# Performance work log

Hardware: AMD Instinct MI355X
Metric: run time of the kernel (lower is better)

Reference implementation:

```python
import jax, jax.numpy as jnp
import numpy as np

EMBED_DIM = 512
N_HEAD = 8
HEAD_DIM = EMBED_DIM // N_HEAD  # 64
B, S = 2, 4096
NEG_FILL = -1e20


def setup_inputs() -> dict:
    key = jax.random.key(0)
    ks = jax.random.split(key, 9)
    inp = {
        "key": jax.random.normal(ks[0], (B, S, EMBED_DIM), jnp.float32),
        "query": jax.random.normal(ks[1], (B, S, EMBED_DIM), jnp.float32),
        "value": jax.random.normal(ks[2], (B, S, EMBED_DIM), jnp.float32),
        "mask": jax.random.randint(ks[3], (1, 1, S, S), 0, 2, jnp.int32),
        # per-head projections (shared across heads, as in the source: a single
        # d x d nn.Linear applied to the last dim of [B,S,H,d])
        "Wq": jax.random.normal(ks[4], (HEAD_DIM, HEAD_DIM), jnp.float32) / np.sqrt(HEAD_DIM),
        "Wk": jax.random.normal(ks[5], (HEAD_DIM, HEAD_DIM), jnp.float32) / np.sqrt(HEAD_DIM),
        "Wv": jax.random.normal(ks[6], (HEAD_DIM, HEAD_DIM), jnp.float32) / np.sqrt(HEAD_DIM),
        "Wo": jax.random.normal(ks[7], (EMBED_DIM, EMBED_DIM), jnp.float32) / np.sqrt(EMBED_DIM),
        "bo": jax.random.normal(ks[8], (EMBED_DIM,), jnp.float32) * 0.01,
    }
    return inp


def reference(key, query, value, mask, Wq, Wk, Wv, Wo, bo):
    b, sq, e = query.shape
    skv = key.shape[1]
    h, d = N_HEAD, HEAD_DIM
    # split heads: [B, S, H, d]
    q = query.reshape(b, sq, h, d) @ Wq.T
    k = key.reshape(b, skv, h, d) @ Wk.T
    v = value.reshape(b, skv, h, d) @ Wv.T
    # scores: [B, H, Sq, Skv]
    scores = jnp.einsum("bqhd,bkhd->bhqk", q, k)
    # source masks BEFORE scaling: fill -1e20 then divide by sqrt(d)
    scores = jnp.where(mask == 0, NEG_FILL, scores)
    scores = scores / np.sqrt(d).astype(np.float32)
    attn = jax.nn.softmax(scores, axis=-1)
    ctx = jnp.einsum("bhqk,bkhd->bqhd", attn, v)  # [B, Sq, H, d]
    concat = ctx.reshape(b, sq, h * d)
    return concat @ Wo.T + bo
```

## Files before the change

### kernel.cpp

```cpp
#include <hip/hip_runtime.h>

typedef __bf16 bf16;
typedef __attribute__((ext_vector_type(8)))  bf16     bf16x8;
typedef __attribute__((ext_vector_type(4)))  bf16     bf16x4;
typedef __attribute__((ext_vector_type(16))) float    f32x16;
typedef __attribute__((ext_vector_type(4)))  float    f32x4;
typedef __attribute__((ext_vector_type(4)))  unsigned uint4v;
typedef __attribute__((ext_vector_type(2)))  unsigned uint2v;

#define SLEN 4096
#define NHEAD 8
#define HDIM 64
#define EMB 512
#define NTILES 64
#define SCALE_LOG2E 0.1803336100254854f

__device__ __forceinline__ f32x16 mfma32(bf16x8 a, bf16x8 b, f32x16 c) {
  return __builtin_amdgcn_mfma_f32_32x32x16_bf16(a, b, c, 0, 0, 0);
}

__device__ __forceinline__ void cp16(const void* g, const void* l) {
  __builtin_amdgcn_global_load_lds(
      (__attribute__((address_space(1))) unsigned int*)(unsigned long long)g,
      (__attribute__((address_space(3))) unsigned int*)(unsigned int)(unsigned long long)l,
      16, 0, 0);
}

__device__ __forceinline__ unsigned pk2(float a, float b) {
  unsigned short ua = __builtin_bit_cast(unsigned short, (bf16)a);
  unsigned short ub = __builtin_bit_cast(unsigned short, (bf16)b);
  return (unsigned)ua | ((unsigned)ub << 16);
}

__global__ __launch_bounds__(256, 2) void proj_qkv(
    const float* __restrict__ key, const float* __restrict__ query, const float* __restrict__ value,
    const float* __restrict__ Wq, const float* __restrict__ Wk, const float* __restrict__ Wv,
    bf16* __restrict__ Qb, bf16* __restrict__ Kb, bf16* __restrict__ VT)
{
  __shared__ __align__(16) bf16 tile[128][64];
  const int tid = threadIdx.x, w = tid >> 6, lane = tid & 63, l31 = lane & 31, lh = lane >> 5;
  const int r0 = blockIdx.x * 128;
  const int m0 = r0 + w * 32;

  #pragma unroll
  for (int p = 0; p < 3; ++p) {
    const float* X = (p == 0) ? query : (p == 1) ? key : value;
    const float* W = (p == 0) ? Wq    : (p == 1) ? Wk  : Wv;

    bf16x8 af[4];
    {
      const float* xr = X + (size_t)(m0 + l31) * 64 + 8 * lh;
      #pragma unroll
      for (int c = 0; c < 4; ++c) {
        f32x4 lo = *(const f32x4*)(xr + c * 16);
        f32x4 hi = *(const f32x4*)(xr + c * 16 + 4);
        bf16x8 v;
        #pragma unroll
        for (int j = 0; j < 4; ++j) { v[j] = (bf16)lo[j]; v[4 + j] = (bf16)hi[j]; }
        af[c] = v;
      }
    }
    bf16x8 bfr[2][4];
    #pragma unroll
    for (int nb = 0; nb < 2; ++nb) {
      const float* wr = W + (size_t)(l31 + 32 * nb) * 64 + 8 * lh;
      #pragma unroll
      for (int c = 0; c < 4; ++c) {
        f32x4 lo = *(const f32x4*)(wr + c * 16);
        f32x4 hi = *(const f32x4*)(wr + c * 16 + 4);
        bf16x8 v;
        #pragma unroll
        for (int j = 0; j < 4; ++j) { v[j] = (bf16)lo[j]; v[4 + j] = (bf16)hi[j]; }
        bfr[nb][c] = v;
      }
    }
    f32x16 a0, a1;
    #pragma unroll
    for (int r = 0; r < 16; ++r) { a0[r] = 0.f; a1[r] = 0.f; }
    #pragma unroll
    for (int c = 0; c < 4; ++c) {
      a0 = mfma32(af[c], bfr[0][c], a0);
      a1 = mfma32(af[c], bfr[1][c], a1);
    }

    __syncthreads();
    #pragma unroll
    for (int r = 0; r < 16; ++r) {
      const int row = w * 32 + (r & 3) + 8 * (r >> 2) + 4 * lh;
      tile[row][l31]      = (bf16)a0[r];
      tile[row][l31 + 32] = (bf16)a1[r];
    }
    __syncthreads();

    if (p < 2) {
      bf16* OUT = p ? Kb : Qb;
      const int rloc = tid >> 1, half = tid & 1;
      const int rg = r0 + rloc, bs = rg >> 3, h = rg & 7, b = bs >> 12, sidx = bs & 4095;
      bf16* dst = OUT + (((size_t)(b * 8 + h) * SLEN + sidx) * 64 + half * 32);
      const bf16* srcp = &tile[rloc][half * 32];
      #pragma unroll
      for (int u = 0; u < 4; ++u) *(uint4v*)(dst + u * 8) = *(const uint4v*)(srcp + u * 8);
    } else {
      const int h = tid >> 5, d0 = tid & 31;
      const int b = blockIdx.x >> 8, s0 = (blockIdx.x * 16) & 4095;
      #pragma unroll
      for (int dh = 0; dh < 2; ++dh) {
        const int dd = d0 + 32 * dh;
        unsigned pk4[8];
        #pragma unroll
        for (int t2 = 0; t2 < 8; ++t2) {
          unsigned short ua = __builtin_bit_cast(unsigned short, tile[(2 * t2) * 8 + h][dd]);
          unsigned short ub = __builtin_bit_cast(unsigned short, tile[(2 * t2 + 1) * 8 + h][dd]);
          pk4[t2] = (unsigned)ua | ((unsigned)ub << 16);
        }
        bf16* dst = VT + ((size_t)(b * 8 + h) * 64 + dd) * SLEN + s0;
        uint4v A; A[0] = pk4[0]; A[1] = pk4[1]; A[2] = pk4[2]; A[3] = pk4[3];
        uint4v Bv; Bv[0] = pk4[4]; Bv[1] = pk4[5]; Bv[2] = pk4[6]; Bv[3] = pk4[7];
        *(uint4v*)(dst) = A;
        *(uint4v*)(dst + 8) = Bv;
      }
    }
  }
}

__device__ __forceinline__ unsigned nib_compress(unsigned x) {
  x = (x | (x >> 4)) & 0x00FF00FFu;
  x = (x | (x >> 8)) & 0x0000FFFFu;
  return x;
}
__global__ void pack_mask(const int* __restrict__ mask, unsigned* __restrict__ MW)
{
  const int w = threadIdx.x >> 6, lane = threadIdx.x & 63;
  const int q = blockIdx.x * 4 + w;
  const int* row = mask + (size_t)q * SLEN;
  unsigned long long mine = 0ull;
  #pragma unroll 4
  for (int i = 0; i < 64; ++i) {
    unsigned long long b = __ballot(row[i * 64 + lane] != 0);
    if (i == lane) mine = b;
  }
  const unsigned lo = (unsigned)mine, hi = (unsigned)(mine >> 32);
  const unsigned w0 = nib_compress(lo & 0x0F0F0F0Fu)        | (nib_compress(hi & 0x0F0F0F0Fu) << 16);
  const unsigned w1 = nib_compress((lo >> 4) & 0x0F0F0F0Fu) | (nib_compress((hi >> 4) & 0x0F0F0F0Fu) << 16);
  MW[(size_t)lane * SLEN + q] = w0;
  MW[(size_t)NTILES * SLEN + (size_t)lane * SLEN + q] = w1;
}

__global__ void wo_split(const float* __restrict__ Wo, bf16* __restrict__ WH, bf16* __restrict__ WL)
{
  const int i = (blockIdx.x * 256 + threadIdx.x) * 4;
  f32x4 v = *(const f32x4*)(Wo + i);
  bf16x4 h, l;
  #pragma unroll
  for (int j = 0; j < 4; ++j) { h[j] = (bf16)v[j]; l[j] = (bf16)(v[j] - (float)h[j]); }
  *(bf16x4*)(WH + i) = h;
  *(bf16x4*)(WL + i) = l;
}

__device__ __forceinline__ void stage_kv4(const bf16* Kb, const bf16* VT, bf16* Kf, bf16* Vf,
                                          int bh, int kv0, int buf, int w, int l31, int lh)
{
  #pragma unroll
  for (int qq = 0; qq < 2; ++qq) {
    const int fid = w * 2 + qq, mb = fid >> 2, c = fid & 3;
    const bf16* ks = Kb + ((size_t)bh * SLEN + kv0 + 32 * mb + l31) * HDIM + c * 16 + 8 * lh;
    cp16(ks, Kf + buf * 4096 + fid * 512);
    const bf16* vs = VT + ((size_t)bh * HDIM + 32 * mb + l31) * SLEN + kv0 + c * 16 + 8 * lh;
    cp16(vs, Vf + buf * 4096 + fid * 512);
  }
}

__global__ __launch_bounds__(256, 4) void attn_kernel(
    const bf16* __restrict__ Qb, const bf16* __restrict__ Kb, const bf16* __restrict__ VT,
    const unsigned* __restrict__ MW,
    bf16* __restrict__ ctxh, bf16* __restrict__ ctxl)
{
  __shared__ __align__(16) unsigned char smem[32768];
  bf16* Kf = (bf16*)smem;
  bf16* Vf = (bf16*)(smem + 16384);

  const int tid = threadIdx.x, w = tid >> 6, lane = tid & 63, l31 = lane & 31, lh = lane >> 5;
  const int qg = w & 1, kc = w >> 1;
  const int bh = blockIdx.x >> 6, qt = blockIdx.x & 63;
  const int q0 = qt * 64;
  const int qrow = q0 + qg * 32 + l31;
  const int lh4 = 4 * lh;

  bf16x8 qf[4];
  {
    const bf16* qp = Qb + ((size_t)bh * SLEN + qrow) * HDIM + 8 * lh;
    #pragma unroll
    for (int c = 0; c < 4; ++c) qf[c] = *(const bf16x8*)(qp + c * 16);
  }

  f32x16 o0, o1;
  #pragma unroll
  for (int r = 0; r < 16; ++r) { o0[r] = 0.f; o1[r] = 0.f; }
  float ls0 = 0.f, ls1 = 0.f, ls2 = 0.f, ls3 = 0.f;

  stage_kv4(Kb, VT, Kf, Vf, bh, 0, 0, w, l31, lh);
  __syncthreads();

  const unsigned* MWl = MW + (size_t)lh * NTILES * SLEN;
  unsigned mw = MWl[qrow];
  for (int t = 0; t < NTILES; ++t) {
    const int cur = t & 1;
    if (t + 1 < NTILES) stage_kv4(Kb, VT, Kf, Vf, bh, (t + 1) * 64, cur ^ 1, w, l31, lh);
    unsigned mwn = 0u;
    if (t + 1 < NTILES) mwn = MWl[(size_t)(t + 1) * SLEN + qrow];

    f32x16 s;
    #pragma unroll
    for (int r = 0; r < 16; ++r) s[r] = 0.f;
    #pragma unroll
    for (int c = 0; c < 4; ++c) {
      bf16x8 a = *(const bf16x8*)(Kf + cur * 4096 + (kc * 4 + c) * 512 + lane * 8);
      s = mfma32(a, qf[c], s);
    }

    const unsigned mwk = mw >> (kc * 16);
    float p[16];
    #pragma unroll
    for (int r = 0; r < 16; ++r) {
      float e = __builtin_amdgcn_exp2f(s[r] * SCALE_LOG2E);
      e *= (float)((mwk >> r) & 1u);
      p[r] = e;
      if      ((r & 3) == 0) ls0 += e;
      else if ((r & 3) == 1) ls1 += e;
      else if ((r & 3) == 2) ls2 += e;
      else                   ls3 += e;
    }

    bf16x8 bp[2];
    #pragma unroll
    for (int cc = 0; cc < 2; ++cc) {
      const int rb = cc * 8;
      unsigned wA0 = pk2(p[rb + 0], p[rb + 1]);
      unsigned wA1 = pk2(p[rb + 2], p[rb + 3]);
      unsigned wB0 = pk2(p[rb + 4], p[rb + 5]);
      unsigned wB1 = pk2(p[rb + 6], p[rb + 7]);
      uint2v r0 = __builtin_amdgcn_permlane32_swap(wA0, wB0, false, false);
      uint2v r1 = __builtin_amdgcn_permlane32_swap(wA1, wB1, false, false);
      uint4v fw; fw[0] = r0[0]; fw[1] = r1[0]; fw[2] = r0[1]; fw[3] = r1[1];
      bp[cc] = __builtin_bit_cast(bf16x8, fw);
    }

    #pragma unroll
    for (int cc = 0; cc < 2; ++cc) {
      bf16x8 v0 = *(const bf16x8*)(Vf + cur * 4096 + (0 * 4 + kc * 2 + cc) * 512 + lane * 8);
      bf16x8 v1 = *(const bf16x8*)(Vf + cur * 4096 + (1 * 4 + kc * 2 + cc) * 512 + lane * 8);
      o0 = mfma32(v0, bp[cc], o0);
      o1 = mfma32(v1, bp[cc], o1);
    }

    __syncthreads();
    mw = mwn;
  }

  float plsum = (ls0 + ls1) + (ls2 + ls3);
  plsum += __shfl_xor(plsum, 32);

  float* PO = (float*)smem;
  float* PL = (float*)(smem + 16384);
  bf16*  Tr = (bf16*)(smem + 17408);

  if (w >= 2) {
    const int pw = w - 2;
    #pragma unroll
    for (int r = 0; r < 16; ++r) {
      PO[(pw * 32 + r) * 64 + lane]      = o0[r];
      PO[(pw * 32 + 16 + r) * 64 + lane] = o1[r];
    }
    PL[pw * 64 + lane] = plsum;
  }
  __syncthreads();

  if (w < 2) {
    #pragma unroll
    for (int r = 0; r < 16; ++r) {
      o0[r] += PO[(w * 32 + r) * 64 + lane];
      o1[r] += PO[(w * 32 + 16 + r) * 64 + lane];
    }
    plsum += PL[w * 64 + lane];
    const float inv = 1.f / plsum;
    #pragma unroll
    for (int r = 0; r < 16; ++r) { o0[r] *= inv; o1[r] *= inv; }
  }
  __syncthreads();

  if (w < 2) {
    #pragma unroll
    for (int r = 0; r < 16; ++r) {
      const int dr = (r & 3) + 8 * (r >> 2) + lh4;
      Tr[(w * 32 + l31) * 72 + dr]      = (bf16)o0[r];
      Tr[(w * 32 + l31) * 72 + 32 + dr] = (bf16)o1[r];
    }
  }
  __syncthreads();
  if (tid < 128) {
    const int rloc = tid >> 1, half = tid & 1;
    bf16* dst = ctxh + ((size_t)bh * SLEN + q0 + rloc) * 64 + half * 32;
    const bf16* srcp = Tr + rloc * 72 + half * 32;
    #pragma unroll
    for (int u = 0; u < 4; ++u) *(uint4v*)(dst + u * 8) = *(const uint4v*)(srcp + u * 8);
  }
  __syncthreads();
  if (w < 2) {
    #pragma unroll
    for (int r = 0; r < 16; ++r) {
      const int dr = (r & 3) + 8 * (r >> 2) + lh4;
      const float h0 = (float)(bf16)o0[r];
      const float h1 = (float)(bf16)o1[r];
      Tr[(w * 32 + l31) * 72 + dr]      = (bf16)(o0[r] - h0);
      Tr[(w * 32 + l31) * 72 + 32 + dr] = (bf16)(o1[r] - h1);
    }
  }
  __syncthreads();
  if (tid < 128) {
    const int rloc = tid >> 1, half = tid & 1;
    bf16* dst = ctxl + ((size_t)bh * SLEN + q0 + rloc) * 64 + half * 32;
    const bf16* srcp = Tr + rloc * 72 + half * 32;
    #pragma unroll
    for (int u = 0; u < 4; ++u) *(uint4v*)(dst + u * 8) = *(const uint4v*)(srcp + u * 8);
  }
}

__global__ __launch_bounds__(256, 2) void out_proj(
    const bf16* __restrict__ CH, const bf16* __restrict__ CL,
    const bf16* __restrict__ WH, const bf16* __restrict__ WL,
    const float* __restrict__ bo, float* __restrict__ out)
{
  __shared__ __align__(16) bf16 Af[2][4][4][64][8];
  const int tid = threadIdx.x, w = tid >> 6, lane = tid & 63, l31 = lane & 31, lh = lane >> 5;
  const int mt = blockIdx.x >> 3, nt = blockIdx.x & 7;
  const int bs0 = mt * 128, n0 = nt * 64;
  const int b = bs0 >> 12, sbase = bs0 & 4095;

  f32x16 a0, a1;
  #pragma unroll
  for (int r = 0; r < 16; ++r) { a0[r] = 0.f; a1[r] = 0.f; }

  for (int kk = 0; kk < 8; ++kk) {
    __syncthreads();
    #pragma unroll
    for (int qq = 0; qq < 8; ++qq) {
      const int fid = w * 8 + qq, pl = fid >> 4, mb = (fid >> 2) & 3, c = fid & 3;
      const bf16* src = (pl ? CL : CH) +
          ((size_t)(b * 8 + kk) * SLEN + sbase + 32 * mb + l31) * 64 + 16 * c + 8 * lh;
      cp16(src, &Af[pl][mb][c][0][0]);
    }
    __syncthreads();

    bf16x8 bh0[4], bl0[4], bh1[4], bl1[4], ah[4], al[4];
    #pragma unroll
    for (int c = 0; c < 4; ++c) {
      const size_t o0off = (size_t)(n0 + l31) * EMB + kk * 64 + 16 * c + 8 * lh;
      const size_t o1off = (size_t)(n0 + l31 + 32) * EMB + kk * 64 + 16 * c + 8 * lh;
      bh0[c] = *(const bf16x8*)(WH + o0off);
      bl0[c] = *(const bf16x8*)(WL + o0off);
      bh1[c] = *(const bf16x8*)(WH + o1off);
      bl1[c] = *(const bf16x8*)(WL + o1off);
      ah[c] = *(const bf16x8*)(&Af[0][w][c][lane][0]);
      al[c] = *(const bf16x8*)(&Af[1][w][c][lane][0]);
    }
    #pragma unroll
    for (int c = 0; c < 4; ++c) {
      a0 = mfma32(ah[c], bh0[c], a0);
      a0 = mfma32(ah[c], bl0[c], a0);
      a0 = mfma32(al[c], bh0[c], a0);
      a1 = mfma32(ah[c], bh1[c], a1);
      a1 = mfma32(ah[c], bl1[c], a1);
      a1 = mfma32(al[c], bh1[c], a1);
    }
  }

  const float bv0 = bo[n0 + l31], bv1 = bo[n0 + l31 + 32];
  #pragma unroll
  for (int r = 0; r < 16; ++r) {
    const int row = bs0 + w * 32 + (r & 3) + 8 * (r >> 2) + 4 * lh;
    out[(size_t)row * EMB + n0 + l31]      = a0[r] + bv0;
    out[(size_t)row * EMB + n0 + l31 + 32] = a1[r] + bv1;
  }
}

extern "C" void kernel_launch(void* const* d_in, const int* in_sizes, int n_in,
                              void* d_out, int out_size, void* d_ws, size_t ws_size,
                              hipStream_t stream)
{
  (void)in_sizes; (void)n_in; (void)out_size; (void)ws_size;
  const float* key   = (const float*)d_in[0];
  const float* query = (const float*)d_in[1];
  const float* value = (const float*)d_in[2];
  const int*   mask  = (const int*)d_in[3];
  const float* Wq    = (const float*)d_in[4];
  const float* Wk    = (const float*)d_in[5];
  const float* Wv    = (const float*)d_in[6];
  const float* Wo    = (const float*)d_in[7];
  const float* bo    = (const float*)d_in[8];
  float* out = (float*)d_out;

  char* ws = (char*)d_ws;
  bf16* Qb = (bf16*)(ws);
  bf16* Kb = (bf16*)(ws + (8ull  << 20));
  bf16* VT = (bf16*)(ws + (16ull << 20));
  unsigned* MW = (unsigned*)(ws + (24ull << 20));
  bf16* CH = (bf16*)(ws + (26ull << 20));
  bf16* CL = (bf16*)(ws + (34ull << 20));
  bf16* WH = (bf16*)(ws + (42ull << 20));
  bf16* WL = (bf16*)(ws + (42ull << 20) + (512ull << 10));

  proj_qkv<<<512, 256, 0, stream>>>(key, query, value, Wq, Wk, Wv, Qb, Kb, VT);
  pack_mask<<<1024, 256, 0, stream>>>(mask, MW);
  wo_split<<<256, 256, 0, stream>>>(Wo, WH, WL);
  attn_kernel<<<1024, 256, 0, stream>>>(Qb, Kb, VT, MW, CH, CL);
  out_proj<<<512, 256, 0, stream>>>(CH, CL, WH, WL, bo, out);
}
```

Measured before the change: 233.8 us.

## Split attention KV range across two blocks and combine partial results

The attention kernel can now split the key/value sequence into two halves processed by separate blocks. Each block writes unnormalised fp32 partial outputs and row sums to workspace, and a new combine kernel merges them into the hi/lo bf16 context. The softmax scale is folded into Q during projection, the mask multiply becomes a bitwise AND, and the tile loop is manually unrolled with pointer increments. The split mode turns on only when the workspace is large enough, and it adds extra global traffic and one more kernel launch.

```diff
diff --git a/kernel.cpp b/kernel.cpp
--- a/kernel.cpp
+++ b/kernel.cpp
@@ -9,7 +9,6 @@
 typedef __attribute__((ext_vector_type(2)))  unsigned uint2v;
 
 #define SLEN 4096
-#define NHEAD 8
 #define HDIM 64
 #define EMB 512
 #define NTILES 64
@@ -83,21 +82,22 @@
       a1 = mfma32(af[c], bfr[1][c], a1);
     }
 
+    const float qs = (p == 0) ? SCALE_LOG2E : 1.0f;
     __syncthreads();
     #pragma unroll
     for (int r = 0; r < 16; ++r) {
       const int row = w * 32 + (r & 3) + 8 * (r >> 2) + 4 * lh;
-      tile[row][l31]      = (bf16)a0[r];
-      tile[row][l31 + 32] = (bf16)a1[r];
+      tile[row][l31]      = (bf16)(a0[r] * qs);
+      tile[row][l31 + 32] = (bf16)(a1[r] * qs);
     }
     __syncthreads();
 
     if (p < 2) {
       bf16* OUT = p ? Kb : Qb;
-      const int rloc = tid >> 1, half = tid & 1;
+      const int rloc = tid >> 1, hf = tid & 1;
       const int rg = r0 + rloc, bs = rg >> 3, h = rg & 7, b = bs >> 12, sidx = bs & 4095;
-      bf16* dst = OUT + (((size_t)(b * 8 + h) * SLEN + sidx) * 64 + half * 32);
-      const bf16* srcp = &tile[rloc][half * 32];
+      bf16* dst = OUT + (((size_t)(b * 8 + h) * SLEN + sidx) * 64 + hf * 32);
+      const bf16* srcp = &tile[rloc][hf * 32];
       #pragma unroll
       for (int u = 0; u < 4; ++u) *(uint4v*)(dst + u * 8) = *(const uint4v*)(srcp + u * 8);
     } else {
@@ -157,171 +157,233 @@
   *(bf16x4*)(WL + i) = l;
 }
 
-__device__ __forceinline__ void stage_kv4(const bf16* Kb, const bf16* VT, bf16* Kf, bf16* Vf,
-                                          int bh, int kv0, int buf, int w, int l31, int lh)
-{
-  #pragma unroll
-  for (int qq = 0; qq < 2; ++qq) {
-    const int fid = w * 2 + qq, mb = fid >> 2, c = fid & 3;
-    const bf16* ks = Kb + ((size_t)bh * SLEN + kv0 + 32 * mb + l31) * HDIM + c * 16 + 8 * lh;
-    cp16(ks, Kf + buf * 4096 + fid * 512);
-    const bf16* vs = VT + ((size_t)bh * HDIM + 32 * mb + l31) * SLEN + kv0 + c * 16 + 8 * lh;
-    cp16(vs, Vf + buf * 4096 + fid * 512);
-  }
-}
-
 __global__ __launch_bounds__(256, 4) void attn_kernel(
     const bf16* __restrict__ Qb, const bf16* __restrict__ Kb, const bf16* __restrict__ VT,
     const unsigned* __restrict__ MW,
-    bf16* __restrict__ ctxh, bf16* __restrict__ ctxl)
+    bf16* __restrict__ ctxh, bf16* __restrict__ ctxl,
+    float* __restrict__ PO, float* __restrict__ PLg, int split)
 {
   __shared__ __align__(16) unsigned char smem[32768];
-  bf16* Kf = (bf16*)smem;
-  bf16* Vf = (bf16*)(smem + 16384);
+  unsigned char* const Ksm = smem;
+  unsigned char* const Vsm = smem + 16384;
 
   const int tid = threadIdx.x, w = tid >> 6, lane = tid & 63, l31 = lane & 31, lh = lane >> 5;
   const int qg = w & 1, kc = w >> 1;
-  const int bh = blockIdx.x >> 6, qt = blockIdx.x & 63;
+  const int half = blockIdx.x >> 10;
+  const int rem = blockIdx.x & 1023;
+  const int bh = rem >> 6, qt = rem & 63;
   const int q0 = qt * 64;
   const int qrow = q0 + qg * 32 + l31;
   const int lh4 = 4 * lh;
-
-  bf16x8 qf[4];
-  {
-    const bf16* qp = Qb + ((size_t)bh * SLEN + qrow) * HDIM + 8 * lh;
-    #pragma unroll
-    for (int c = 0; c < 4; ++c) qf[c] = *(const bf16x8*)(qp + c * 16);
-  }
-
-  f32x16 o0, o1;
-  #pragma unroll
-  for (int r = 0; r < 16; ++r) { o0[r] = 0.f; o1[r] = 0.f; }
-  float ls0 = 0.f, ls1 = 0.f, ls2 = 0.f, ls3 = 0.f;
-
-  stage_kv4(Kb, VT, Kf, Vf, bh, 0, 0, w, l31, lh);
+  const int kcs = kc << 4;
+  const int ntiles = (split == 2) ? 32 : 64;
+  const int kt0 = half * 32;
+
+  const bf16* qp = Qb + ((size_t)bh * SLEN + qrow) * HDIM + 8 * lh;
+  const bf16x8 qf0 = *(const bf16x8*)(qp);
+  const bf16x8 qf1 = *(const bf16x8*)(qp + 16);
+  const bf16x8 qf2 = *(const bf16x8*)(qp + 32);
+  const bf16x8 qf3 = *(const bf16x8*)(qp + 48);
+
+  const int f0 = 2 * w, f1 = 2 * w + 1;
+  const bf16* kp0 = Kb + ((size_t)bh * SLEN + kt0 * 64 + (f0 >> 2) * 32 + l31) * HDIM + (f0 & 3) * 16 + 8 * lh;
+  const bf16* kp1 = Kb + ((size_t)bh * SLEN + kt0 * 64 + (f1 >> 2) * 32 + l31) * HDIM + (f1 & 3) * 16 + 8 * lh;
+  const bf16* vp0 = VT + ((size_t)bh * HDIM + (f0 >> 2) * 32 + l31) * SLEN + kt0 * 64 + (f0 & 3) * 16 + 8 * lh;
+  const bf16* vp1 = VT + ((size_t)bh * HDIM + (f1 >> 2) * 32 + l31) * SLEN + kt0 * 64 + (f1 & 3) * 16 + 8 * lh;
+  unsigned char* const dk0 = Ksm + f0 * 1024;
+  unsigned char* const dv0 = Vsm + f0 * 1024;
+
+  const int lb = lane * 16;
+  const unsigned char* kr = Ksm + kc * 4096 + lb;
+  const unsigned char* vr = Vsm + kc * 2048 + lb;
+
+  f32x16 o0, o1, Z16;
+  #pragma unroll
+  for (int r = 0; r < 16; ++r) { o0[r] = 0.f; o1[r] = 0.f; Z16[r] = 0.f; }
+  float la0 = 0.f, la1 = 0.f, la2 = 0.f, la3 = 0.f;
+
+  cp16(kp0, dk0); cp16(kp1, dk0 + 1024); cp16(vp0, dv0); cp16(vp1, dv0 + 1024);
+  kp0 += 4096; kp1 += 4096; vp0 += 64; vp1 += 64;
+  const unsigned* mp = MW + (size_t)lh * NTILES * SLEN + (size_t)kt0 * SLEN + qrow;
+  unsigned mwc = *mp;
   __syncthreads();
 
-  const unsigned* MWl = MW + (size_t)lh * NTILES * SLEN;
-  unsigned mw = MWl[qrow];
-  for (int t = 0; t < NTILES; ++t) {
-    const int cur = t & 1;
-    if (t + 1 < NTILES) stage_kv4(Kb, VT, Kf, Vf, bh, (t + 1) * 64, cur ^ 1, w, l31, lh);
-    unsigned mwn = 0u;
-    if (t + 1 < NTILES) mwn = MWl[(size_t)(t + 1) * SLEN + qrow];
-
-    f32x16 s;
-    #pragma unroll
-    for (int r = 0; r < 16; ++r) s[r] = 0.f;
-    #pragma unroll
-    for (int c = 0; c < 4; ++c) {
-      bf16x8 a = *(const bf16x8*)(Kf + cur * 4096 + (kc * 4 + c) * 512 + lane * 8);
-      s = mfma32(a, qf[c], s);
-    }
-
-    const unsigned mwk = mw >> (kc * 16);
-    float p[16];
-    #pragma unroll
-    for (int r = 0; r < 16; ++r) {
-      float e = __builtin_amdgcn_exp2f(s[r] * SCALE_LOG2E);
-      e *= (float)((mwk >> r) & 1u);
-      p[r] = e;
-      if      ((r & 3) == 0) ls0 += e;
-      else if ((r & 3) == 1) ls1 += e;
-      else if ((r & 3) == 2) ls2 += e;
-      else                   ls3 += e;
-    }
-
-    bf16x8 bp[2];
-    #pragma unroll
-    for (int cc = 0; cc < 2; ++cc) {
-      const int rb = cc * 8;
-      unsigned wA0 = pk2(p[rb + 0], p[rb + 1]);
-      unsigned wA1 = pk2(p[rb + 2], p[rb + 3]);
-      unsigned wB0 = pk2(p[rb + 4], p[rb + 5]);
-      unsigned wB1 = pk2(p[rb + 6], p[rb + 7]);
-      uint2v r0 = __builtin_amdgcn_permlane32_swap(wA0, wB0, false, false);
-      uint2v r1 = __builtin_amdgcn_permlane32_swap(wA1, wB1, false, false);
-      uint4v fw; fw[0] = r0[0]; fw[1] = r1[0]; fw[2] = r0[1]; fw[3] = r1[1];
-      bp[cc] = __builtin_bit_cast(bf16x8, fw);
-    }
-
-    #pragma unroll
-    for (int cc = 0; cc < 2; ++cc) {
-      bf16x8 v0 = *(const bf16x8*)(Vf + cur * 4096 + (0 * 4 + kc * 2 + cc) * 512 + lane * 8);
-      bf16x8 v1 = *(const bf16x8*)(Vf + cur * 4096 + (1 * 4 + kc * 2 + cc) * 512 + lane * 8);
-      o0 = mfma32(v0, bp[cc], o0);
-      o1 = mfma32(v1, bp[cc], o1);
-    }
-
-    __syncthreads();
-    mw = mwn;
-  }
-
-  float plsum = (ls0 + ls1) + (ls2 + ls3);
+#define LDK(B, C)      (*(const bf16x8*)(kr + (B) * 8192 + (C) * 1024))
+#define LDV(B, MB, CC) (*(const bf16x8*)(vr + (B) * 8192 + (MB) * 4096 + (CC) * 1024))
+
+#define TILE(B, MWCUR, MWNXT) { \
+  MWNXT = mp[SLEN]; mp += SLEN; \
+  cp16(kp0, dk0 + (1 - (B)) * 8192); cp16(kp1, dk0 + (1 - (B)) * 8192 + 1024); \
+  cp16(vp0, dv0 + (1 - (B)) * 8192); cp16(vp1, dv0 + (1 - (B)) * 8192 + 1024); \
+  kp0 += 4096; kp1 += 4096; vp0 += 64; vp1 += 64; \
+  f32x16 s = mfma32(LDK(B, 0), qf0, Z16); \
+  s = mfma32(LDK(B, 1), qf1, s); \
+  s = mfma32(LDK(B, 2), qf2, s); \
+  s = mfma32(LDK(B, 3), qf3, s); \
+  const unsigned mwk = (MWCUR) >> kcs; \
+  float p[16]; \
+  _Pragma("unroll") \
+  for (int r = 0; r < 16; ++r) { \
+    float e = __builtin_amdgcn_exp2f(s[r]); \
+    unsigned kbit = (unsigned)(((int)(mwk << (31 - r))) >> 31); \
+    e = __builtin_bit_cast(float, __builtin_bit_cast(unsigned, e) & kbit); \
+    p[r] = e; \
+    if ((r & 3) == 0) la0 += e; else if ((r & 3) == 1) la1 += e; \
+    else if ((r & 3) == 2) la2 += e; else la3 += e; \
+  } \
+  _Pragma("unroll") \
+  for (int b = 0; b < 2; ++b) { \
+    unsigned Wa = pk2(p[8 * b + 0], p[8 * b + 1]); \
+    unsigned Wb = pk2(p[8 * b + 2], p[8 * b + 3]); \
+    unsigned Wc = pk2(p[8 * b + 4], p[8 * b + 5]); \
+    unsigned Wd = pk2(p[8 * b + 6], p[8 * b + 7]); \
+    uint2v s02 = __builtin_amdgcn_permlane32_swap(Wa, Wc, false, false); \
+    uint2v s13 = __builtin_amdgcn_permlane32_swap(Wb, Wd, false, false); \
+    uint4v fw; fw[0] = s02[0]; fw[1] = s13[0]; fw[2] = s02[1]; fw[3] = s13[1]; \
+    const bf16x8 bp = __builtin_bit_cast(bf16x8, fw); \
+    o0 = mfma32(LDV(B, 0, b), bp, o0); \
+    o1 = mfma32(LDV(B, 1, b), bp, o1); \
+  } \
+  __syncthreads(); \
+}
+
+  const int pairs = ntiles >> 1;
+  unsigned mwn;
+  for (int tp = 0; tp < pairs; ++tp) {
+    TILE(0, mwc, mwn)
+    TILE(1, mwn, mwc)
+  }
+#undef LDK
+#undef LDV
+#undef TILE
+
+  float plsum = (la0 + la1) + (la2 + la3);
   plsum += __shfl_xor(plsum, 32);
 
-  float* PO = (float*)smem;
-  float* PL = (float*)(smem + 16384);
-  bf16*  Tr = (bf16*)(smem + 17408);
+  float* POl = (float*)smem;
+  float* PLl = (float*)(smem + 16384);
 
   if (w >= 2) {
     const int pw = w - 2;
     #pragma unroll
     for (int r = 0; r < 16; ++r) {
-      PO[(pw * 32 + r) * 64 + lane]      = o0[r];
-      PO[(pw * 32 + 16 + r) * 64 + lane] = o1[r];
-    }
-    PL[pw * 64 + lane] = plsum;
-  }
-  __syncthreads();
-
-  if (w < 2) {
-    #pragma unroll
-    for (int r = 0; r < 16; ++r) {
-      o0[r] += PO[(w * 32 + r) * 64 + lane];
-      o1[r] += PO[(w * 32 + 16 + r) * 64 + lane];
-    }
-    plsum += PL[w * 64 + lane];
-    const float inv = 1.f / plsum;
-    #pragma unroll
-    for (int r = 0; r < 16; ++r) { o0[r] *= inv; o1[r] *= inv; }
-  }
-  __syncthreads();
-
-  if (w < 2) {
-    #pragma unroll
-    for (int r = 0; r < 16; ++r) {
-      const int dr = (r & 3) + 8 * (r >> 2) + lh4;
-      Tr[(w * 32 + l31) * 72 + dr]      = (bf16)o0[r];
-      Tr[(w * 32 + l31) * 72 + 32 + dr] = (bf16)o1[r];
-    }
-  }
-  __syncthreads();
-  if (tid < 128) {
-    const int rloc = tid >> 1, half = tid & 1;
-    bf16* dst = ctxh + ((size_t)bh * SLEN + q0 + rloc) * 64 + half * 32;
-    const bf16* srcp = Tr + rloc * 72 + half * 32;
-    #pragma unroll
-    for (int u = 0; u < 4; ++u) *(uint4v*)(dst + u * 8) = *(const uint4v*)(srcp + u * 8);
+      POl[(pw * 32 + r) * 64 + lane]      = o0[r];
+      POl[(pw * 32 + 16 + r) * 64 + lane] = o1[r];
+    }
+    PLl[pw * 64 + lane] = plsum;
   }
   __syncthreads();
   if (w < 2) {
     #pragma unroll
     for (int r = 0; r < 16; ++r) {
-      const int dr = (r & 3) + 8 * (r >> 2) + lh4;
-      const float h0 = (float)(bf16)o0[r];
-      const float h1 = (float)(bf16)o1[r];
-      Tr[(w * 32 + l31) * 72 + dr]      = (bf16)(o0[r] - h0);
-      Tr[(w * 32 + l31) * 72 + 32 + dr] = (bf16)(o1[r] - h1);
-    }
-  }
-  __syncthreads();
-  if (tid < 128) {
-    const int rloc = tid >> 1, half = tid & 1;
-    bf16* dst = ctxl + ((size_t)bh * SLEN + q0 + rloc) * 64 + half * 32;
-    const bf16* srcp = Tr + rloc * 72 + half * 32;
-    #pragma unroll
-    for (int u = 0; u < 4; ++u) *(uint4v*)(dst + u * 8) = *(const uint4v*)(srcp + u * 8);
+      o0[r] += POl[(w * 32 + r) * 64 + lane];
+      o1[r] += POl[(w * 32 + 16 + r) * 64 + lane];
+    }
+    plsum += PLl[w * 64 + lane];
+  }
+
+  if (split == 1) {
+    if (w < 2) {
+      const float inv = 1.f / plsum;
+      #pragma unroll
+      for (int r = 0; r < 16; ++r) { o0[r] *= inv; o1[r] *= inv; }
+    }
+    __syncthreads();
+
+    bf16* Tr = (bf16*)(smem + 17408);
+    if (w < 2) {
+      #pragma unroll
+      for (int r = 0; r < 16; ++r) {
+        const int dr = (r & 3) + 8 * (r >> 2) + lh4;
+        Tr[(w * 32 + l31) * 72 + dr]      = (bf16)o0[r];
+        Tr[(w * 32 + l31) * 72 + 32 + dr] = (bf16)o1[r];
+      }
+    }
+    __syncthreads();
+    if (tid < 128) {
+      const int rloc = tid >> 1, hf = tid & 1;
+      bf16* dst = ctxh + ((size_t)bh * SLEN + q0 + rloc) * 64 + hf * 32;
+      const bf16* srcp = Tr + rloc * 72 + hf * 32;
+      #pragma unroll
+      for (int u = 0; u < 4; ++u) *(uint4v*)(dst + u * 8) = *(const uint4v*)(srcp + u * 8);
+    }
+    __syncthreads();
+    if (w < 2) {
+      #pragma unroll
+      for (int r = 0; r < 16; ++r) {
+        const int dr = (r & 3) + 8 * (r >> 2) + lh4;
+        const float h0 = (float)(bf16)o0[r];
+        const float h1 = (float)(bf16)o1[r];
+        Tr[(w * 32 + l31) * 72 + dr]      = (bf16)(o0[r] - h0);
+        Tr[(w * 32 + l31) * 72 + 32 + dr] = (bf16)(o1[r] - h1);
+      }
+    }
+    __syncthreads();
+    if (tid < 128) {
+      const int rloc = tid >> 1, hf = tid & 1;
+      bf16* dst = ctxl + ((size_t)bh * SLEN + q0 + rloc) * 64 + hf * 32;
+      const bf16* srcp = Tr + rloc * 72 + hf * 32;
+      #pragma unroll
+      for (int u = 0; u < 4; ++u) *(uint4v*)(dst + u * 8) = *(const uint4v*)(srcp + u * 8);
+    }
+  } else {
+    __syncthreads();
+    float* Trf = (float*)smem;
+    float* PLs = (float*)(smem + 17408);
+    if (w < 2) {
+      #pragma unroll
+      for (int r = 0; r < 16; ++r) {
+        const int dr = (r & 3) + 8 * (r >> 2) + lh4;
+        Trf[(w * 32 + l31) * 68 + dr]      = o0[r];
+        Trf[(w * 32 + l31) * 68 + 32 + dr] = o1[r];
+      }
+      if (lh == 0) PLs[w * 32 + l31] = plsum;
+    }
+    __syncthreads();
+    const int qq = tid >> 2, part = tid & 3;
+    float* dst = PO + ((size_t)(half * 16 + bh) * SLEN + q0 + qq) * 64 + part * 16;
+    const float* srcp = Trf + qq * 68 + part * 16;
+    #pragma unroll
+    for (int u = 0; u < 4; ++u) *(f32x4*)(dst + u * 4) = *(const f32x4*)(srcp + u * 4);
+    if (tid < 64) PLg[(size_t)(half * 16 + bh) * SLEN + q0 + tid] = PLs[tid];
+  }
+}
+
+__global__ __launch_bounds__(256) void combine_halves(
+    const float* __restrict__ PO, const float* __restrict__ PLg,
+    bf16* __restrict__ CH, bf16* __restrict__ CL)
+{
+  const int bh = blockIdx.x >> 5, qt = blockIdx.x & 31;
+  const int t = threadIdx.x;
+  const int q = qt * 128 + (t >> 1);
+  const size_t HOFF = (size_t)16 * SLEN * 64;
+  const size_t base = ((size_t)bh * SLEN + q) * 64 + (t & 1) * 32;
+  const float inv = 1.f / (PLg[(size_t)bh * SLEN + q] +
+                           PLg[(size_t)16 * SLEN + (size_t)bh * SLEN + q]);
+  const float* p0 = PO + base;
+  const float* p1 = PO + HOFF + base;
+  unsigned hw[16], lw[16];
+  #pragma unroll
+  for (int i = 0; i < 8; ++i) {
+    f32x4 a = *(const f32x4*)(p0 + i * 4);
+    f32x4 b = *(const f32x4*)(p1 + i * 4);
+    float v0 = (a[0] + b[0]) * inv, v1 = (a[1] + b[1]) * inv;
+    float v2 = (a[2] + b[2]) * inv, v3 = (a[3] + b[3]) * inv;
+    float h0 = (float)(bf16)v0, h1 = (float)(bf16)v1;
+    float h2 = (float)(bf16)v2, h3 = (float)(bf16)v3;
+    hw[i * 2]     = pk2(v0, v1);
+    hw[i * 2 + 1] = pk2(v2, v3);
+    lw[i * 2]     = pk2(v0 - h0, v1 - h1);
+    lw[i * 2 + 1] = pk2(v2 - h2, v3 - h3);
+  }
+  bf16* ch = CH + base;
+  bf16* cl = CL + base;
+  #pragma unroll
+  for (int u = 0; u < 4; ++u) {
+    uint4v H; H[0] = hw[u*4]; H[1] = hw[u*4+1]; H[2] = hw[u*4+2]; H[3] = hw[u*4+3];
+    uint4v L; L[0] = lw[u*4]; L[1] = lw[u*4+1]; L[2] = lw[u*4+2]; L[3] = lw[u*4+3];
+    *(uint4v*)(ch + u * 8) = H;
+    *(uint4v*)(cl + u * 8) = L;
   }
 }
 
@@ -387,7 +449,7 @@
                               void* d_out, int out_size, void* d_ws, size_t ws_size,
                               hipStream_t stream)
 {
-  (void)in_sizes; (void)n_in; (void)out_size; (void)ws_size;
+  (void)in_sizes; (void)n_in; (void)out_size;
   const float* key   = (const float*)d_in[0];
   const float* query = (const float*)d_in[1];
   const float* value = (const float*)d_in[2];
@@ -408,10 +470,16 @@
   bf16* CL = (bf16*)(ws + (34ull << 20));
   bf16* WH = (bf16*)(ws + (42ull << 20));
   bf16* WL = (bf16*)(ws + (42ull << 20) + (512ull << 10));
+  float* PO  = (float*)(ws + (44ull << 20));
+  float* PLg = (float*)(ws + (78ull << 20));
+
+  const size_t need_split = (78ull << 20) + (2ull * 16 * SLEN * 4);
+  const int split = (ws_size >= need_split) ? 2 : 1;
 
   proj_qkv<<<512, 256, 0, stream>>>(key, query, value, Wq, Wk, Wv, Qb, Kb, VT);
   pack_mask<<<1024, 256, 0, stream>>>(mask, MW);
   wo_split<<<256, 256, 0, stream>>>(Wo, WH, WL);
-  attn_kernel<<<1024, 256, 0, stream>>>(Qb, Kb, VT, MW, CH, CL);
+  attn_kernel<<<1024 * split, 256, 0, stream>>>(Qb, Kb, VT, MW, CH, CL, PO, PLg, split);
+  if (split == 2) combine_halves<<<512, 256, 0, stream>>>(PO, PLg, CH, CL);
   out_proj<<<512, 256, 0, stream>>>(CH, CL, WH, WL, bo, out);
 }
```

Measured after the change: 249.5 us. +6.7%, slower.

## Triple-buffer K/V staging with one barrier per tile and prescaled Q

Applied to the files above, without the earlier changes.

The attention kernel moves from double to triple buffering of K/V tiles in LDS. Loads are issued two tiles ahead, and a partial vmcnt wait plus a single s_barrier replaces the end-of-iteration __syncthreads. The softmax scale times log2e is folded into Q at projection time, and the mask is applied with a bitwise AND instead of a float multiply. MFMA sections get raised wave priority. LDS use grows to 48KB and occupancy hint drops from 4 to 3 blocks per CU, which risks losing latency hiding. Folding the scale into Q before bf16 rounding slightly changes numerics.

```diff
diff --git a/kernel.cpp b/kernel.cpp
--- a/kernel.cpp
+++ b/kernel.cpp
@@ -9,7 +9,6 @@
 typedef __attribute__((ext_vector_type(2)))  unsigned uint2v;
 
 #define SLEN 4096
-#define NHEAD 8
 #define HDIM 64
 #define EMB 512
 #define NTILES 64
@@ -83,21 +82,22 @@
       a1 = mfma32(af[c], bfr[1][c], a1);
     }
 
+    const float qs = (p == 0) ? SCALE_LOG2E : 1.0f;
     __syncthreads();
     #pragma unroll
     for (int r = 0; r < 16; ++r) {
       const int row = w * 32 + (r & 3) + 8 * (r >> 2) + 4 * lh;
-      tile[row][l31]      = (bf16)a0[r];
-      tile[row][l31 + 32] = (bf16)a1[r];
+      tile[row][l31]      = (bf16)(a0[r] * qs);
+      tile[row][l31 + 32] = (bf16)(a1[r] * qs);
     }
     __syncthreads();
 
     if (p < 2) {
       bf16* OUT = p ? Kb : Qb;
-      const int rloc = tid >> 1, half = tid & 1;
+      const int rloc = tid >> 1, hf = tid & 1;
       const int rg = r0 + rloc, bs = rg >> 3, h = rg & 7, b = bs >> 12, sidx = bs & 4095;
-      bf16* dst = OUT + (((size_t)(b * 8 + h) * SLEN + sidx) * 64 + half * 32);
-      const bf16* srcp = &tile[rloc][half * 32];
+      bf16* dst = OUT + (((size_t)(b * 8 + h) * SLEN + sidx) * 64 + hf * 32);
+      const bf16* srcp = &tile[rloc][hf * 32];
       #pragma unroll
       for (int u = 0; u < 4; ++u) *(uint4v*)(dst + u * 8) = *(const uint4v*)(srcp + u * 8);
     } else {
@@ -157,27 +157,12 @@
   *(bf16x4*)(WL + i) = l;
 }
 
-__device__ __forceinline__ void stage_kv4(const bf16* Kb, const bf16* VT, bf16* Kf, bf16* Vf,
-                                          int bh, int kv0, int buf, int w, int l31, int lh)
-{
-  #pragma unroll
-  for (int qq = 0; qq < 2; ++qq) {
-    const int fid = w * 2 + qq, mb = fid >> 2, c = fid & 3;
-    const bf16* ks = Kb + ((size_t)bh * SLEN + kv0 + 32 * mb + l31) * HDIM + c * 16 + 8 * lh;
-    cp16(ks, Kf + buf * 4096 + fid * 512);
-    const bf16* vs = VT + ((size_t)bh * HDIM + 32 * mb + l31) * SLEN + kv0 + c * 16 + 8 * lh;
-    cp16(vs, Vf + buf * 4096 + fid * 512);
-  }
-}
-
-__global__ __launch_bounds__(256, 4) void attn_kernel(
+__global__ __launch_bounds__(256, 3) void attn_kernel(
     const bf16* __restrict__ Qb, const bf16* __restrict__ Kb, const bf16* __restrict__ VT,
     const unsigned* __restrict__ MW,
     bf16* __restrict__ ctxh, bf16* __restrict__ ctxl)
 {
-  __shared__ __align__(16) unsigned char smem[32768];
-  bf16* Kf = (bf16*)smem;
-  bf16* Vf = (bf16*)(smem + 16384);
+  __shared__ __align__(16) unsigned char smem[49152];
 
   const int tid = threadIdx.x, w = tid >> 6, lane = tid & 63, l31 = lane & 31, lh = lane >> 5;
   const int qg = w & 1, kc = w >> 1;
@@ -185,109 +170,141 @@
   const int q0 = qt * 64;
   const int qrow = q0 + qg * 32 + l31;
   const int lh4 = 4 * lh;
-
-  bf16x8 qf[4];
-  {
-    const bf16* qp = Qb + ((size_t)bh * SLEN + qrow) * HDIM + 8 * lh;
-    #pragma unroll
-    for (int c = 0; c < 4; ++c) qf[c] = *(const bf16x8*)(qp + c * 16);
-  }
-
-  f32x16 o0, o1;
+  const int kcs = kc << 4;
+
+  const bf16* qp = Qb + ((size_t)bh * SLEN + qrow) * HDIM + 8 * lh;
+  const bf16x8 qf0 = *(const bf16x8*)(qp);
+  const bf16x8 qf1 = *(const bf16x8*)(qp + 16);
+  const bf16x8 qf2 = *(const bf16x8*)(qp + 32);
+  const bf16x8 qf3 = *(const bf16x8*)(qp + 48);
+
+  const int f0 = 2 * w, f1 = 2 * w + 1;
+  const bf16* kp0 = Kb + ((size_t)bh * SLEN + (f0 >> 2) * 32 + l31) * HDIM + (f0 & 3) * 16 + 8 * lh;
+  const bf16* kp1 = Kb + ((size_t)bh * SLEN + (f1 >> 2) * 32 + l31) * HDIM + (f1 & 3) * 16 + 8 * lh;
+  const bf16* vp0 = VT + ((size_t)bh * HDIM + (f0 >> 2) * 32 + l31) * SLEN + (f0 & 3) * 16 + 8 * lh;
+  const bf16* vp1 = VT + ((size_t)bh * HDIM + (f1 >> 2) * 32 + l31) * SLEN + (f1 & 3) * 16 + 8 * lh;
+
+  unsigned char* sA = smem;
+  unsigned char* sB = smem + 16384;
+  unsigned char* sC = smem + 32768;
+  const int fko = f0 * 1024;
+  const int fvo = 8192 + f0 * 1024;
+  const int lb = lane * 16;
+  const int kroff = kc * 4096 + lb;
+  const int vroff = 8192 + kc * 2048 + lb;
+
+  f32x16 o0, o1, Z16;
   #pragma unroll
-  for (int r = 0; r < 16; ++r) { o0[r] = 0.f; o1[r] = 0.f; }
-  float ls0 = 0.f, ls1 = 0.f, ls2 = 0.f, ls3 = 0.f;
-
-  stage_kv4(Kb, VT, Kf, Vf, bh, 0, 0, w, l31, lh);
-  __syncthreads();
-
-  const unsigned* MWl = MW + (size_t)lh * NTILES * SLEN;
-  unsigned mw = MWl[qrow];
+  for (int r = 0; r < 16; ++r) { o0[r] = 0.f; o1[r] = 0.f; Z16[r] = 0.f; }
+  float la0 = 0.f, la1 = 0.f, la2 = 0.f, la3 = 0.f;
+
+  const unsigned* mp = MW + (size_t)lh * NTILES * SLEN + qrow;
+
+  cp16(kp0, sA + fko); cp16(kp1, sA + fko + 1024);
+  cp16(vp0, sA + fvo); cp16(vp1, sA + fvo + 1024);
+  kp0 += 4096; kp1 += 4096; vp0 += 64; vp1 += 64;
+  unsigned mwc = *mp;
+  mp += SLEN;
+  cp16(kp0, sB + fko); cp16(kp1, sB + fko + 1024);
+  cp16(vp0, sB + fvo); cp16(vp1, sB + fvo + 1024);
+  kp0 += 4096; kp1 += 4096; vp0 += 64; vp1 += 64;
+
   for (int t = 0; t < NTILES; ++t) {
-    const int cur = t & 1;
-    if (t + 1 < NTILES) stage_kv4(Kb, VT, Kf, Vf, bh, (t + 1) * 64, cur ^ 1, w, l31, lh);
-    unsigned mwn = 0u;
-    if (t + 1 < NTILES) mwn = MWl[(size_t)(t + 1) * SLEN + qrow];
-
-    f32x16 s;
-    #pragma unroll
-    for (int r = 0; r < 16; ++r) s[r] = 0.f;
-    #pragma unroll
-    for (int c = 0; c < 4; ++c) {
-      bf16x8 a = *(const bf16x8*)(Kf + cur * 4096 + (kc * 4 + c) * 512 + lane * 8);
-      s = mfma32(a, qf[c], s);
-    }
-
-    const unsigned mwk = mw >> (kc * 16);
+    asm volatile("s_waitcnt vmcnt(4)" ::: "memory");
+    __builtin_amdgcn_sched_barrier(0);
+    __builtin_amdgcn_s_barrier();
+
+    const unsigned mwn = *mp;
+    mp += SLEN;
+
+    cp16(kp0, sC + fko); cp16(kp1, sC + fko + 1024);
+    cp16(vp0, sC + fvo); cp16(vp1, sC + fvo + 1024);
+    kp0 += 4096; kp1 += 4096; vp0 += 64; vp1 += 64;
+
+    const unsigned char* kr = sA + kroff;
+    const unsigned char* vr = sA + vroff;
+
+    __builtin_amdgcn_s_setprio(1);
+    f32x16 s = mfma32(*(const bf16x8*)(kr), qf0, Z16);
+    s = mfma32(*(const bf16x8*)(kr + 1024), qf1, s);
+    s = mfma32(*(const bf16x8*)(kr + 2048), qf2, s);
+    s = mfma32(*(const bf16x8*)(kr + 3072), qf3, s);
+    __builtin_amdgcn_s_setprio(0);
+
+    const unsigned mwk = mwc >> kcs;
     float p[16];
     #pragma unroll
     for (int r = 0; r < 16; ++r) {
-      float e = __builtin_amdgcn_exp2f(s[r] * SCALE_LOG2E);
-      e *= (float)((mwk >> r) & 1u);
+      float e = __builtin_amdgcn_exp2f(s[r]);
+      unsigned kbit = (unsigned)(((int)(mwk << (31 - r))) >> 31);
+      e = __builtin_bit_cast(float, __builtin_bit_cast(unsigned, e) & kbit);
       p[r] = e;
-      if      ((r & 3) == 0) ls0 += e;
-      else if ((r & 3) == 1) ls1 += e;
-      else if ((r & 3) == 2) ls2 += e;
-      else                   ls3 += e;
-    }
-
-    bf16x8 bp[2];
-    #pragma unroll
-    for (int cc = 0; cc < 2; ++cc) {
-      const int rb = cc * 8;
-      unsigned wA0 = pk2(p[rb + 0], p[rb + 1]);
-      unsigned wA1 = pk2(p[rb + 2], p[rb + 3]);
-      unsigned wB0 = pk2(p[rb + 4], p[rb + 5]);
-      unsigned wB1 = pk2(p[rb + 6], p[rb + 7]);
-      uint2v r0 = __builtin_amdgcn_permlane32_swap(wA0, wB0, false, false);
-      uint2v r1 = __builtin_amdgcn_permlane32_swap(wA1, wB1, false, false);
-      uint4v fw; fw[0] = r0[0]; fw[1] = r1[0]; fw[2] = r0[1]; fw[3] = r1[1];
-      bp[cc] = __builtin_bit_cast(bf16x8, fw);
-    }
-
-    #pragma unroll
-    for (int cc = 0; cc < 2; ++cc) {
-      bf16x8 v0 = *(const bf16x8*)(Vf + cur * 4096 + (0 * 4 + kc * 2 + cc) * 512 + lane * 8);
-      bf16x8 v1 = *(const bf16x8*)(Vf + cur * 4096 + (1 * 4 + kc * 2 + cc) * 512 + lane * 8);
-      o0 = mfma32(v0, bp[cc], o0);
-      o1 = mfma32(v1, bp[cc], o1);
-    }
-
-    __syncthreads();
-    mw = mwn;
-  }
-
-  float plsum = (ls0 + ls1) + (ls2 + ls3);
+      if ((r & 3) == 0) la0 += e; else if ((r & 3) == 1) la1 += e;
+      else if ((r & 3) == 2) la2 += e; else la3 += e;
+    }
+
+    bf16x8 bp0, bp1;
+    {
+      unsigned Wa = pk2(p[0], p[1]), Wb = pk2(p[2], p[3]);
+      unsigned Wc = pk2(p[4], p[5]), Wd = pk2(p[6], p[7]);
+      uint2v s02 = __builtin_amdgcn_permlane32_swap(Wa, Wc, false, false);
+      uint2v s13 = __builtin_amdgcn_permlane32_swap(Wb, Wd, false, false);
+      uint4v fw; fw[0] = s02[0]; fw[1] = s13[0]; fw[2] = s02[1]; fw[3] = s13[1];
+      bp0 = __builtin_bit_cast(bf16x8, fw);
+    }
+    {
+      unsigned Wa = pk2(p[8], p[9]), Wb = pk2(p[10], p[11]);
+      unsigned Wc = pk2(p[12], p[13]), Wd = pk2(p[14], p[15]);
+      uint2v s02 = __builtin_amdgcn_permlane32_swap(Wa, Wc, false, false);
+      uint2v s13 = __builtin_amdgcn_permlane32_swap(Wb, Wd, false, false);
+      uint4v fw; fw[0] = s02[0]; fw[1] = s13[0]; fw[2] = s02[1]; fw[3] = s13[1];
+      bp1 = __builtin_bit_cast(bf16x8, fw);
+    }
+
+    __builtin_amdgcn_s_setprio(1);
+    o0 = mfma32(*(const bf16x8*)(vr), bp0, o0);
+    o0 = mfma32(*(const bf16x8*)(vr + 1024), bp1, o0);
+    o1 = mfma32(*(const bf16x8*)(vr + 4096), bp0, o1);
+    o1 = mfma32(*(const bf16x8*)(vr + 4096 + 1024), bp1, o1);
+    __builtin_amdgcn_s_setprio(0);
+
+    { unsigned char* tmp_ = sA; sA = sB; sB = sC; sC = tmp_; }
+    mwc = mwn;
+  }
+
+  asm volatile("s_waitcnt vmcnt(0)" ::: "memory");
+  __builtin_amdgcn_s_barrier();
+
+  float plsum = (la0 + la1) + (la2 + la3);
   plsum += __shfl_xor(plsum, 32);
 
-  float* PO = (float*)smem;
-  float* PL = (float*)(smem + 16384);
-  bf16*  Tr = (bf16*)(smem + 17408);
+  float* POl = (float*)smem;
+  float* PLl = (float*)(smem + 16384);
 
   if (w >= 2) {
     const int pw = w - 2;
     #pragma unroll
     for (int r = 0; r < 16; ++r) {
-      PO[(pw * 32 + r) * 64 + lane]      = o0[r];
-      PO[(pw * 32 + 16 + r) * 64 + lane] = o1[r];
-    }
-    PL[pw * 64 + lane] = plsum;
+      POl[(pw * 32 + r) * 64 + lane]      = o0[r];
+      POl[(pw * 32 + 16 + r) * 64 + lane] = o1[r];
+    }
+    PLl[pw * 64 + lane] = plsum;
   }
   __syncthreads();
-
   if (w < 2) {
     #pragma unroll
     for (int r = 0; r < 16; ++r) {
-      o0[r] += PO[(w * 32 + r) * 64 + lane];
-      o1[r] += PO[(w * 32 + 16 + r) * 64 + lane];
-    }
-    plsum += PL[w * 64 + lane];
+      o0[r] += POl[(w * 32 + r) * 64 + lane];
+      o1[r] += POl[(w * 32 + 16 + r) * 64 + lane];
+    }
+    plsum += PLl[w * 64 + lane];
     const float inv = 1.f / plsum;
     #pragma unroll
     for (int r = 0; r < 16; ++r) { o0[r] *= inv; o1[r] *= inv; }
   }
   __syncthreads();
 
+  bf16* Tr = (bf16*)(smem + 17408);
   if (w < 2) {
     #pragma unroll
     for (int r = 0; r < 16; ++r) {
@@ -298,9 +315,9 @@
   }
   __syncthreads();
   if (tid < 128) {
-    const int rloc = tid >> 1, half = tid & 1;
-    bf16* dst = ctxh + ((size_t)bh * SLEN + q0 + rloc) * 64 + half * 32;
-    const bf16* srcp = Tr + rloc * 72 + half * 32;
+    const int rloc = tid >> 1, hf = tid & 1;
+    bf16* dst = ctxh + ((size_t)bh * SLEN + q0 + rloc) * 64 + hf * 32;
+    const bf16* srcp = Tr + rloc * 72 + hf * 32;
     #pragma unroll
     for (int u = 0; u < 4; ++u) *(uint4v*)(dst + u * 8) = *(const uint4v*)(srcp + u * 8);
   }
@@ -317,9 +334,9 @@
   }
   __syncthreads();
   if (tid < 128) {
-    const int rloc = tid >> 1, half = tid & 1;
-    bf16* dst = ctxl + ((size_t)bh * SLEN + q0 + rloc) * 64 + half * 32;
-    const bf16* srcp = Tr + rloc * 72 + half * 32;
+    const int rloc = tid >> 1, hf = tid & 1;
+    bf16* dst = ctxl + ((size_t)bh * SLEN + q0 + rloc) * 64 + hf * 32;
+    const bf16* srcp = Tr + rloc * 72 + hf * 32;
     #pragma unroll
     for (int u = 0; u < 4; ++u) *(uint4v*)(dst + u * 8) = *(const uint4v*)(srcp + u * 8);
   }
```

After: 268.0 us. 14.6% more time.
